# Performance work log

Measured on AMD Instinct MI355X. Metric: run time of the kernel, lower is better.

Reference implementation:

```python
import jax, jax.numpy as jnp
import numpy as np

H_LSTM = 80          # span-encoder LSTM hidden
SPAN_DIM = 4 * H_LSTM  # 320
ADU_DIM = 256        # han_out_size
HEADS = 3
HAN_HID = 256
CTX_DIM = 200


def lstm(x, W_ih, W_hh, b, reverse=False):
    # x: [T, B, In] -> hidden states [T, B, H]; torch gate order i,f,g,o
    H = W_hh.shape[1]
    B = x.shape[1]

    def step(carry, xt):
        h, c = carry
        z = xt @ W_ih.T + h @ W_hh.T + b
        i, f, g, o = jnp.split(z, 4, axis=-1)
        c = jax.nn.sigmoid(f) * c + jax.nn.sigmoid(i) * jnp.tanh(g)
        h = jax.nn.sigmoid(o) * jnp.tanh(c)
        return (h, c), h

    init = (jnp.zeros((B, H), x.dtype), jnp.zeros((B, H), x.dtype))
    _, hs = jax.lax.scan(step, init, x, reverse=reverse)
    return hs


def span_rep(seq, spans):
    # seq [L, 2H], spans [..., 2] -> [..., 4H]
    f, bwd = seq[:, :H_LSTM], seq[:, H_LSTM:]
    i, j = spans[..., 0], spans[..., 1]
    fi1, fj = f[i - 1], f[j]
    bi, bj1 = bwd[i], bwd[j + 1]
    return jnp.concatenate([fj - fi1, bi - bj1, fi1, bj1], axis=-1)


def gat_metapath(h, src, dst, emask, W, a_l, a_r, bias):
    # single-metapath GATConv (dgl semantics): h [A, Din], W [K, Din, D]
    A = h.shape[0]
    hp = jnp.einsum('ad,kdo->ako', h, W)  # [A,K,D]
    e = jax.nn.leaky_relu(jnp.einsum('eko,ko->ek', hp[src], a_l)
                          + jnp.einsum('eko,ko->ek', hp[dst], a_r), 0.2)
    e = jnp.where(emask[:, None], e, -1e9)
    m = jax.ops.segment_max(e, dst, num_segments=A)           # [A,K]
    ex = jnp.where(emask[:, None], jnp.exp(e - m[dst]), 0.0)
    den = jax.ops.segment_sum(ex, dst, num_segments=A)
    alpha = ex / jnp.maximum(den[dst], 1e-9)                  # edge softmax per dst
    out = jax.ops.segment_sum(alpha[:, :, None] * hp[src], dst, num_segments=A)
    out = jax.nn.elu(out + bias)                              # [A,K,D]
    return out.reshape(A, -1)                                 # [A, K*D]


def attn_pool(feats, vals, mask, W1, b1, W2, b2):
    # tiny MLP -> Softmax over axis 0 over the kept (masked) set
    s = jnp.maximum(feats @ W1 + b1, 0.0) @ W2 + b2           # [N,1]
    s = jnp.where(mask[:, None], s, -1e9)
    a = jnp.where(mask[:, None], jax.nn.softmax(s, axis=0), 0.0)
    out = (a * vals).sum(0)
    return jnp.where(mask.any(), out, jnp.zeros_like(out))


def _forward(token_embed, info_scores,
             Wih_f, Whh_f, b_f, Wih_b, Whh_b, b_b,
             W_gat, a_l, a_r, b_gat, W_sem, b_sem, q_sem, W_pred, b_pred,
             W_adu1, b_adu1, W_adu2, b_adu2,
             W_inn1, b_inn1, W_inn2, b_inn2,
             W_int1, b_int1, W_int2, b_int2,
             Wih_c, Whh_c, b_c,
             comment_spans, adu_spans, adu_masks, local_masks,
             inner_src, inner_dst, inner_rel, inner_mask,
             inter_src, inter_dst, inter_rel, inter_mask):
    # bidirectional span encoder over frozen LF token embeddings
    x = token_embed.transpose(1, 0, 2)                        # [L, C, 768]
    hf = lstm(x, Wih_f, Whh_f, b_f)
    hb = lstm(x, Wih_b, Whh_b, b_b, reverse=True)
    span_enc = jnp.concatenate([hf, hb], -1).transpose(1, 0, 2)  # [C, L, 2H]

    def per_comment(seq, cspan, aspans, amask, lmask,
                    isrc, idst, irel, imask_e,
                    tsrc, tdst, trel, tmask_e, info):
        cemb = span_rep(seq, cspan)                           # [320]
        adus = span_rep(seq, aspans) * amask[:, None]         # [A, 320]
        A = adus.shape[0]
        # meta-paths: inner Attack, inner Support, inter AttackedBy(rev), inter SupportedBy(rev)
        srcs = jnp.stack([isrc, isrc, tdst, tdst])
        dsts = jnp.stack([idst, idst, tsrc, tsrc])
        masks = jnp.stack([imask_e & (irel == 0), imask_e & (irel == 1),
                           tmask_e & (trel == 0), tmask_e & (trel == 1)])
        z = jax.vmap(gat_metapath, in_axes=(None, 0, 0, 0, 0, 0, 0, 0))(
            adus, srcs, dsts, masks, W_gat, a_l, a_r, b_gat)  # [4, A, K*D]
        # semantic attention across meta-paths (masked mean over real nodes)
        w = jnp.tanh(z @ W_sem + b_sem) @ q_sem               # [4, A]
        w = (w * amask[None, :]).sum(1) / jnp.maximum(amask.sum(), 1)
        beta = jax.nn.softmax(w)                              # [4]
        zfin = jnp.einsum('m,mad->ad', beta, z)               # [A, K*D]
        adu_embeds = zfin @ W_pred + b_pred                   # [A, 256]
        # ADU attention pooling over locally-used ADUs
        feats = jnp.concatenate(
            [jnp.broadcast_to(cemb, (A, SPAN_DIM)), adu_embeds], -1)
        attended_adu = attn_pool(feats, adu_embeds, amask & lmask,
                                 W_adu1, b_adu1, W_adu2, b_adu2)

        def pair_attend(se, de, rel, me, W1, b1, W2, b2):
            # relation lut: Attack(0)->[0,1], Support(1)->[1,0]
            onehot = jnp.stack([rel, 1 - rel], -1).astype(adu_embeds.dtype)
            pe = jnp.concatenate([adu_embeds[se], adu_embeds[de], onehot], -1)  # [E,514]
            fp = jnp.concatenate(
                [jnp.broadcast_to(cemb, (pe.shape[0], SPAN_DIM)), pe], -1)
            return attn_pool(fp, pe, me, W1, b1, W2, b2)

        attended_inner = pair_attend(isrc, idst, irel, imask_e,
                                     W_inn1, b_inn1, W_inn2, b_inn2)
        # revert_inter_post_relations=True: embed = cat(emb[pair1], emb[pair0], rel)
        attended_inter = pair_attend(tdst, tsrc, trel, tmask_e,
                                     W_int1, b_int1, W_int2, b_int2)
        return jnp.concatenate([attended_adu, attended_inner, attended_inter,
                                info, cemb])                  # [1608]

    wo_ctx = jax.vmap(per_comment)(span_enc, comment_spans, adu_spans, adu_masks,
                                   local_masks, inner_src, inner_dst, inner_rel,
                                   inner_mask, inter_src, inter_dst, inter_rel,
                                   inter_mask, info_scores)   # [C, 1608]
    # comment compressor LSTM along the comment sequence (batch = 1)
    ctx = lstm(wo_ctx[:, None, :], Wih_c, Whh_c, b_c)[:, 0, :]  # [C, 200]
    return jnp.concatenate([ctx, wo_ctx], -1)                 # [C, 1808]


def setup_inputs():
    C, L, A, E, INFO = 64, 1024, 32, 48, 4
    key = jax.random.key(0)
    ks = iter(jax.random.split(key, 64))
    rng = np.random.default_rng(0)

    def u(shape):  # uniform init as in _weight_init, scaled for stability
        return jax.random.uniform(next(ks), shape, jnp.float32, -0.1, 0.1)

    token_embed = jax.random.normal(next(ks), (C, L, 768), jnp.float32)
    info_scores = jax.random.normal(next(ks), (C, INFO), jnp.float32)
    ci = rng.integers(1, L // 2, C)
    cj = rng.integers(L // 2, L - 2, C)
    comment_spans = jnp.stack([jnp.asarray(ci), jnp.asarray(cj)], 1).astype(jnp.int32)
    ai = rng.integers(1, L - 40, (C, A))
    adu_spans = jnp.stack([jnp.asarray(ai), jnp.asarray(ai + rng.integers(1, 30, (C, A)))], -1).astype(jnp.int32)
    adu_masks = jnp.ones((C, A), jnp.bool_)
    local_masks = jnp.asarray(rng.integers(0, 2, (C, A)) > 0)
    ei = lambda hi, shp: jnp.asarray(rng.integers(0, hi, shp), jnp.int32)
    eb = lambda shp: jnp.asarray(rng.integers(0, 2, shp) > 0)
    inp = dict(token_embed=token_embed, info_scores=info_scores,
               comment_spans=comment_spans, adu_spans=adu_spans,
               adu_masks=adu_masks, local_masks=local_masks,
               inner_src=ei(A, (C, E)), inner_dst=ei(A, (C, E)),
               inner_rel=ei(2, (C, E)), inner_mask=eb((C, E)),
               inter_src=ei(A, (C, E)), inter_dst=ei(A, (C, E)),
               inter_rel=ei(2, (C, E)), inter_mask=eb((C, E)))
    D_WO = SPAN_DIM + ADU_DIM * 5 + 4 + INFO  # 1608
    params = dict(
        Wih_f=u((4 * H_LSTM, 768)), Whh_f=u((4 * H_LSTM, H_LSTM)), b_f=u((4 * H_LSTM,)),
        Wih_b=u((4 * H_LSTM, 768)), Whh_b=u((4 * H_LSTM, H_LSTM)), b_b=u((4 * H_LSTM,)),
        W_gat=u((4, HEADS, SPAN_DIM, HAN_HID)), a_l=u((4, HEADS, HAN_HID)),
        a_r=u((4, HEADS, HAN_HID)), b_gat=u((4, HEADS, HAN_HID)),
        W_sem=u((HEADS * HAN_HID, 128)), b_sem=u((128,)), q_sem=u((128,)),
        W_pred=u((HEADS * HAN_HID, ADU_DIM)), b_pred=u((ADU_DIM,)),
        W_adu1=u((SPAN_DIM + ADU_DIM, 16)), b_adu1=u((16,)), W_adu2=u((16, 1)), b_adu2=u((1,)),
        W_inn1=u((SPAN_DIM + 2 * ADU_DIM + 2, 16)), b_inn1=u((16,)), W_inn2=u((16, 1)), b_inn2=u((1,)),
        W_int1=u((SPAN_DIM + 2 * ADU_DIM + 2, 16)), b_int1=u((16,)), W_int2=u((16, 1)), b_int2=u((1,)),
        Wih_c=u((4 * CTX_DIM, D_WO)), Whh_c=u((4 * CTX_DIM, CTX_DIM)), b_c=u((4 * CTX_DIM,)))
    inp.update(params)
    return inp


def reference(token_embed, info_scores,
              Wih_f, Whh_f, b_f, Wih_b, Whh_b, b_b,
              W_gat, a_l, a_r, b_gat, W_sem, b_sem, q_sem, W_pred, b_pred,
              W_adu1, b_adu1, W_adu2, b_adu2,
              W_inn1, b_inn1, W_inn2, b_inn2,
              W_int1, b_int1, W_int2, b_int2,
              Wih_c, Whh_c, b_c,
              comment_spans, adu_spans, adu_masks, local_masks,
              inner_src, inner_dst, inner_rel, inner_mask,
              inter_src, inter_dst, inter_rel, inter_mask):
    return _forward(token_embed, info_scores,
                    Wih_f, Whh_f, b_f, Wih_b, Whh_b, b_b,
                    W_gat, a_l, a_r, b_gat, W_sem, b_sem, q_sem, W_pred, b_pred,
                    W_adu1, b_adu1, W_adu2, b_adu2,
                    W_inn1, b_inn1, W_inn2, b_inn2,
                    W_int1, b_int1, W_int2, b_int2,
                    Wih_c, Whh_c, b_c,
                    comment_spans, adu_spans, adu_masks, local_masks,
                    inner_src, inner_dst, inner_rel, inner_mask,
                    inter_src, inter_dst, inter_rel, inter_mask)
```

## Files before the change

kernel.cpp:

```cpp
#include <hip/hip_runtime.h>
#include <hip/hip_bf16.h>
#include <hip/hip_fp16.h>
#include <stdint.h>

typedef unsigned int u32;
typedef unsigned short u16;
typedef __attribute__((ext_vector_type(8))) short short8;
typedef __attribute__((ext_vector_type(4))) float f32x4;
typedef _Float16 half2v __attribute__((ext_vector_type(2)));

#if defined(__has_builtin)
#if __has_builtin(__builtin_amdgcn_fdot2)
#define HAVE_FDOT2 1
#endif
#endif

__device__ __forceinline__ float bf2f_u(u32 lo16) { return __uint_as_float(lo16 << 16); }
__device__ __forceinline__ u32 f2bf_bits(float x) {
  u32 u = __float_as_uint(x);
  return (u + 0x7fffu + ((u >> 16) & 1u)) >> 16;
}
__device__ __forceinline__ u32 pk2bf(float x, float y) {
  return f2bf_bits(x) | (f2bf_bits(y) << 16);
}
__device__ __forceinline__ u32 pk2bf_tr(float x, float y) {
  return (__float_as_uint(y) & 0xffff0000u) | (__float_as_uint(x) >> 16);
}
__device__ __forceinline__ u32 pkh(float x, float y) {
  return (u32)__half_as_ushort(__float2half(x)) |
         ((u32)__half_as_ushort(__float2half(y)) << 16);
}
__device__ __forceinline__ float dot2h(u32 w, u32 h, float acc) {
#ifdef HAVE_FDOT2
  return __builtin_amdgcn_fdot2(__builtin_bit_cast(half2v, w), __builtin_bit_cast(half2v, h),
                                acc, false);
#else
  union { u32 u; __half2 h2; } uw, uh;
  uw.u = w; uh.u = h;
  float2 wf = __half22float2(uw.h2);
  float2 hf = __half22float2(uh.h2);
  return acc + wf.x * hf.x + wf.y * hf.y;
#endif
}
__device__ __forceinline__ float sigf(float x) { return 1.0f / (1.0f + __expf(-x)); }
__device__ __forceinline__ float tanhf_fast(float x) {
  float ax = fabsf(x);
  float e = __expf(-2.0f * ax);
  float t = (1.0f - e) / (1.0f + e);
  return x < 0.0f ? -t : t;
}
__device__ __forceinline__ float eluf(float x) { return x > 0.0f ? x : __expf(x) - 1.0f; }
__device__ __forceinline__ float lreluf(float x) { return x > 0.0f ? x : 0.2f * x; }

__device__ __forceinline__ int maskmode(const void* am) { return (*(const u32*)am) > 0xFFu; }
__device__ __forceinline__ int ldmask(const void* p, int i, int mb) {
  return mb ? (int)((const unsigned char*)p)[i] : ((const int*)p)[i];
}

__global__ void k_marker(float* out) { out[0] = 12345.0f; }

__global__ void k_prep(const float* __restrict__ Wgat, const float* __restrict__ al,
                       const float* __restrict__ ar, float* __restrict__ alproj,
                       float* __restrict__ arproj) {
  int idx = blockIdx.x * 256 + threadIdx.x;
  if (idx >= 3840) return;
  int mk = idx / 320, d = idx % 320;
  const float* wrow = Wgat + ((size_t)mk * 320 + d) * 256;
  const float* alp = al + mk * 256;
  const float* arp = ar + mk * 256;
  float sa = 0.f, sb = 0.f;
  for (int o = 0; o < 256; ++o) {
    float w = wrow[o];
    sa += w * alp[o];
    sb += w * arp[o];
  }
  alproj[idx] = sa;
  arproj[idx] = sb;
}

__global__ void k_pack(const float* __restrict__ whhc, uint4* __restrict__ wt4) {
  int idx = blockIdx.x * 256 + threadIdx.x;
  if (idx >= 20000) return;
  int k4 = idx / 800, r = idx % 800;
  const float* p = whhc + r * 200 + k4 * 8;
  wt4[idx] = (uint4){pkh(p[0], p[1]), pkh(p[2], p[3]), pkh(p[4], p[5]), pkh(p[6], p[7])};
}

__global__ void k_packemb(const float* __restrict__ emb, u32* __restrict__ dst) {
  const float4* s = (const float4*)emb;
  uint2* d = (uint2*)dst;
  const int n = 12582912;
  for (int i = blockIdx.x * blockDim.x + threadIdx.x; i < n; i += gridDim.x * blockDim.x) {
    float4 v = s[i];
    d[i] = (uint2){pk2bf_tr(v.x, v.y), pk2bf_tr(v.z, v.w)};
  }
}

__global__ void k_packw(const float* __restrict__ Wf, const float* __restrict__ Wb,
                        u32* __restrict__ dst) {
  int idx = blockIdx.x * 256 + threadIdx.x;
  if (idx >= 245760) return;
  int n = idx / 384, q = (idx % 384) * 2;
  const float* src = (n < 320) ? (Wf + (size_t)n * 768) : (Wb + (size_t)(n - 320) * 768);
  dst[idx] = pk2bf_tr(src[q], src[q + 1]);
}

__global__ __launch_bounds__(256) void k_gemm_in(
    const float* __restrict__ emb, const float* __restrict__ Wf, const float* __restrict__ Wb,
    const float* __restrict__ biasf, const float* __restrict__ biasb, float* __restrict__ Z) {
  __shared__ u16 Albs[128 * 40];
  __shared__ u16 Blbs[128 * 40];
  __shared__ float bias_l[128];
  const int tid = threadIdx.x;
  const int n0 = blockIdx.x * 128;
  const int m0 = blockIdx.y * 128;

  if (tid < 128) {
    int ng = n0 + tid;
    bias_l[tid] = (ng < 320) ? biasf[ng] : biasb[ng - 320];
  }
  const int srow = tid >> 1, shalf = tid & 1;
  const float* asrc = emb + (size_t)(m0 + srow) * 768 + shalf * 16;
  const int ngb = n0 + srow;
  const float* bsrc =
      ((ngb < 320) ? (Wf + (size_t)ngb * 768) : (Wb + (size_t)(ngb - 320) * 768)) + shalf * 16;
  u32* aw = (u32*)&Albs[srow * 40 + shalf * 16];
  u32* bw = (u32*)&Blbs[srow * 40 + shalf * 16];

  const int lane = tid & 63;
  const int lr = lane & 15, sub = lane >> 4;
  const int wv = tid >> 6, wm = wv >> 1, wn = wv & 1;
  const u16* abase = &Albs[(wm * 64 + lr) * 40 + sub * 8];
  const u16* bbase = &Blbs[(wn * 64 + lr) * 40 + sub * 8];

  f32x4 acc[4][4];
#pragma unroll
  for (int i = 0; i < 4; ++i)
#pragma unroll
    for (int j = 0; j < 4; ++j) acc[i][j] = (f32x4)(0.f);

  float4 a0, a1, a2, a3, b0, b1, b2, b3;
  u32 pra[8], prb[8];
  a0 = *(const float4*)(asrc + 0); a1 = *(const float4*)(asrc + 4);
  a2 = *(const float4*)(asrc + 8); a3 = *(const float4*)(asrc + 12);
  b0 = *(const float4*)(bsrc + 0); b1 = *(const float4*)(bsrc + 4);
  b2 = *(const float4*)(bsrc + 8); b3 = *(const float4*)(bsrc + 12);
  pra[0] = pk2bf_tr(a0.x, a0.y); pra[1] = pk2bf_tr(a0.z, a0.w);
  pra[2] = pk2bf_tr(a1.x, a1.y); pra[3] = pk2bf_tr(a1.z, a1.w);
  pra[4] = pk2bf_tr(a2.x, a2.y); pra[5] = pk2bf_tr(a2.z, a2.w);
  pra[6] = pk2bf_tr(a3.x, a3.y); pra[7] = pk2bf_tr(a3.z, a3.w);
  prb[0] = pk2bf_tr(b0.x, b0.y); prb[1] = pk2bf_tr(b0.z, b0.w);
  prb[2] = pk2bf_tr(b1.x, b1.y); prb[3] = pk2bf_tr(b1.z, b1.w);
  prb[4] = pk2bf_tr(b2.x, b2.y); prb[5] = pk2bf_tr(b2.z, b2.w);
  prb[6] = pk2bf_tr(b3.x, b3.y); prb[7] = pk2bf_tr(b3.z, b3.w);

  for (int it = 0; it < 24; ++it) {
    __syncthreads();
#pragma unroll
    for (int q = 0; q < 8; ++q) { aw[q] = pra[q]; bw[q] = prb[q]; }
    __syncthreads();
    const bool more = (it + 1 < 24);
    if (more) {
      const int k0 = (it + 1) * 32;
      a0 = *(const float4*)(asrc + k0); a1 = *(const float4*)(asrc + k0 + 4);
      a2 = *(const float4*)(asrc + k0 + 8); a3 = *(const float4*)(asrc + k0 + 12);
      b0 = *(const float4*)(bsrc + k0); b1 = *(const float4*)(bsrc + k0 + 4);
      b2 = *(const float4*)(bsrc + k0 + 8); b3 = *(const float4*)(bsrc + k0 + 12);
    }
    short8 bfr[4];
#pragma unroll
    for (int nf = 0; nf < 4; ++nf) bfr[nf] = *(const short8*)(bbase + nf * 640);
#pragma unroll
    for (int mf = 0; mf < 4; ++mf) {
      short8 af = *(const short8*)(abase + mf * 640);
#pragma unroll
      for (int nf = 0; nf < 4; ++nf)
        acc[mf][nf] = __builtin_amdgcn_mfma_f32_16x16x32_bf16(af, bfr[nf], acc[mf][nf], 0, 0, 0);
    }
    if (more) {
      pra[0] = pk2bf_tr(a0.x, a0.y); pra[1] = pk2bf_tr(a0.z, a0.w);
      pra[2] = pk2bf_tr(a1.x, a1.y); pra[3] = pk2bf_tr(a1.z, a1.w);
      pra[4] = pk2bf_tr(a2.x, a2.y); pra[5] = pk2bf_tr(a2.z, a2.w);
      pra[6] = pk2bf_tr(a3.x, a3.y); pra[7] = pk2bf_tr(a3.z, a3.w);
      prb[0] = pk2bf_tr(b0.x, b0.y); prb[1] = pk2bf_tr(b0.z, b0.w);
      prb[2] = pk2bf_tr(b1.x, b1.y); prb[3] = pk2bf_tr(b1.z, b1.w);
      prb[4] = pk2bf_tr(b2.x, b2.y); prb[5] = pk2bf_tr(b2.z, b2.w);
      prb[6] = pk2bf_tr(b3.x, b3.y); prb[7] = pk2bf_tr(b3.z, b3.w);
    }
  }
#pragma unroll
  for (int mf = 0; mf < 4; ++mf) {
#pragma unroll
    for (int nf = 0; nf < 4; ++nf) {
      int col = wn * 64 + nf * 16 + lr;
      float bias = bias_l[col];
      size_t mrow = (size_t)m0 + wm * 64 + mf * 16 + sub * 4;
#pragma unroll
      for (int j = 0; j < 4; ++j)
        Z[(mrow + j) * 640 + n0 + col] = acc[mf][nf][j] + bias;
    }
  }
}

__global__ __launch_bounds__(256) void k_gemm_in2(
    const u32* __restrict__ ebf, const u32* __restrict__ wbf, const float* __restrict__ biasf,
    const float* __restrict__ biasb, float* __restrict__ Z) {
  __shared__ u16 Albs[128 * 40];
  __shared__ u16 Blbs[128 * 40];
  __shared__ float bias_l[128];
  const int tid = threadIdx.x;
  const int n0 = blockIdx.x * 128;
  const int m0 = blockIdx.y * 128;

  if (tid < 128) {
    int ng = n0 + tid;
    bias_l[tid] = (ng < 320) ? biasf[ng] : biasb[ng - 320];
  }
  const int srow = tid >> 1, shalf = tid & 1;
  const uint4* ea = (const uint4*)ebf + (size_t)(m0 + srow) * 96 + shalf * 2;
  const uint4* eb = (const uint4*)wbf + (size_t)(n0 + srow) * 96 + shalf * 2;
  uint4* aw4 = (uint4*)&Albs[srow * 40 + shalf * 16];
  uint4* bw4 = (uint4*)&Blbs[srow * 40 + shalf * 16];

  const int lane = tid & 63;
  const int lr = lane & 15, sub = lane >> 4;
  const int wv = tid >> 6, wm = wv >> 1, wn = wv & 1;
  const u16* abase = &Albs[(wm * 64 + lr) * 40 + sub * 8];
  const u16* bbase = &Blbs[(wn * 64 + lr) * 40 + sub * 8];

  f32x4 acc[4][4];
#pragma unroll
  for (int i = 0; i < 4; ++i)
#pragma unroll
    for (int j = 0; j < 4; ++j) acc[i][j] = (f32x4)(0.f);

  uint4 pa0 = ea[0], pa1 = ea[1], pb0 = eb[0], pb1 = eb[1];
  for (int it = 0; it < 24; ++it) {
    __syncthreads();
    aw4[0] = pa0; aw4[1] = pa1;
    bw4[0] = pb0; bw4[1] = pb1;
    __syncthreads();
    if (it + 1 < 24) {
      pa0 = ea[(it + 1) * 4]; pa1 = ea[(it + 1) * 4 + 1];
      pb0 = eb[(it + 1) * 4]; pb1 = eb[(it + 1) * 4 + 1];
    }
    short8 bfr[4];
#pragma unroll
    for (int nf = 0; nf < 4; ++nf) bfr[nf] = *(const short8*)(bbase + nf * 640);
#pragma unroll
    for (int mf = 0; mf < 4; ++mf) {
      short8 af = *(const short8*)(abase + mf * 640);
#pragma unroll
      for (int nf = 0; nf < 4; ++nf)
        acc[mf][nf] = __builtin_amdgcn_mfma_f32_16x16x32_bf16(af, bfr[nf], acc[mf][nf], 0, 0, 0);
    }
  }
#pragma unroll
  for (int mf = 0; mf < 4; ++mf) {
#pragma unroll
    for (int nf = 0; nf < 4; ++nf) {
      int col = wn * 64 + nf * 16 + lr;
      float bias = bias_l[col];
      size_t mrow = (size_t)m0 + wm * 64 + mf * 16 + sub * 4;
#pragma unroll
      for (int j = 0; j < 4; ++j)
        Z[(mrow + j) * 640 + n0 + col] = acc[mf][nf][j] + bias;
    }
  }
}

__global__ __launch_bounds__(320, 1) void k_lstm_tok(const float* __restrict__ Z,
                                                     const float* __restrict__ Whhf,
                                                     const float* __restrict__ Whhb,
                                                     float* __restrict__ hf,
                                                     float* __restrict__ hb) {
  __shared__ uint2 wq[20 * 320];
  __shared__ alignas(16) u32 hpkA[40];
  __shared__ alignas(16) u32 hpkB[40];
  const int tid = threadIdx.x;
  const int c = blockIdx.x >> 1;
  const int dir = blockIdx.x & 1;
  const float* Whh = dir ? Whhb : Whhf;
  float* hout = dir ? hb : hf;

  for (int idx = tid; idx < 20 * 320; idx += 320) {
    int k4 = idx / 320, r = idx % 320;
    const float* p = Whh + (size_t)r * 80 + k4 * 4;
    wq[idx] = (uint2){pkh(p[0], p[1]), pkh(p[2], p[3])};
  }
  if (tid < 40) hpkA[tid] = 0;
  __syncthreads();

  const int u = tid >> 2, g = tid & 3;
  const int r = g * 80 + u;
  const int lb = tid & 60;
  const uint2* wcol = wq + r;
  uint2 wv0 = wcol[0], wv1 = wcol[320], wv2 = wcol[640], wv3 = wcol[960];
  uint2 wv4 = wcol[1280], wv5 = wcol[1600], wv6 = wcol[1920], wv7 = wcol[2240];
  uint2 wv8 = wcol[2560], wv9 = wcol[2880], wv10 = wcol[3200], wv11 = wcol[3520];
  uint2 wv12 = wcol[3840], wv13 = wcol[4160], wv14 = wcol[4480], wv15 = wcol[4800];
  uint2 wv16 = wcol[5120], wv17 = wcol[5440], wv18 = wcol[5760], wv19 = wcol[6080];
  asm volatile("" : "+v"(wv0.x), "+v"(wv0.y), "+v"(wv1.x), "+v"(wv1.y), "+v"(wv2.x),
                    "+v"(wv2.y), "+v"(wv3.x), "+v"(wv3.y), "+v"(wv4.x), "+v"(wv4.y),
                    "+v"(wv5.x), "+v"(wv5.y), "+v"(wv6.x), "+v"(wv6.y), "+v"(wv7.x),
                    "+v"(wv7.y), "+v"(wv8.x), "+v"(wv8.y), "+v"(wv9.x), "+v"(wv9.y));
  asm volatile("" : "+v"(wv10.x), "+v"(wv10.y), "+v"(wv11.x), "+v"(wv11.y), "+v"(wv12.x),
                    "+v"(wv12.y), "+v"(wv13.x), "+v"(wv13.y), "+v"(wv14.x), "+v"(wv14.y),
                    "+v"(wv15.x), "+v"(wv15.y), "+v"(wv16.x), "+v"(wv16.y), "+v"(wv17.x),
                    "+v"(wv17.y), "+v"(wv18.x), "+v"(wv18.y), "+v"(wv19.x), "+v"(wv19.y));

  const int sgn = dir ? -1 : 1;
  const int t0 = dir ? 1023 : 0;
  const float* zb = Z + (size_t)c * 1024 * 640 + dir * 320 + r;
  float zc = zb[(size_t)t0 * 640];
  float zn = zb[(size_t)(t0 + sgn) * 640];
  float cst = 0.f;
  const u32* cur = hpkA;
  u32* nxt = hpkB;
  float* hbase = hout + (size_t)c * 1024 * 80 + u;

  for (int t = 0; t < 1024; ++t) {
    const int tt = t0 + sgn * t;
    float zp = 0.f;
    if (t + 2 < 1024) zp = zb[(size_t)(t0 + sgn * (t + 2)) * 640];
    float a0 = zc, a1 = 0.f, a2 = 0.f, a3 = 0.f;
    {
      uint4 h0 = *(const uint4*)&cur[0];
      a0 = dot2h(wv0.x, h0.x, a0); a1 = dot2h(wv0.y, h0.y, a1);
      a2 = dot2h(wv1.x, h0.z, a2); a3 = dot2h(wv1.y, h0.w, a3);
      uint4 h1 = *(const uint4*)&cur[4];
      a0 = dot2h(wv2.x, h1.x, a0); a1 = dot2h(wv2.y, h1.y, a1);
      a2 = dot2h(wv3.x, h1.z, a2); a3 = dot2h(wv3.y, h1.w, a3);
      uint4 h2 = *(const uint4*)&cur[8];
      a0 = dot2h(wv4.x, h2.x, a0); a1 = dot2h(wv4.y, h2.y, a1);
      a2 = dot2h(wv5.x, h2.z, a2); a3 = dot2h(wv5.y, h2.w, a3);
      uint4 h3 = *(const uint4*)&cur[12];
      a0 = dot2h(wv6.x, h3.x, a0); a1 = dot2h(wv6.y, h3.y, a1);
      a2 = dot2h(wv7.x, h3.z, a2); a3 = dot2h(wv7.y, h3.w, a3);
      uint4 h4 = *(const uint4*)&cur[16];
      a0 = dot2h(wv8.x, h4.x, a0); a1 = dot2h(wv8.y, h4.y, a1);
      a2 = dot2h(wv9.x, h4.z, a2); a3 = dot2h(wv9.y, h4.w, a3);
      uint4 h5 = *(const uint4*)&cur[20];
      a0 = dot2h(wv10.x, h5.x, a0); a1 = dot2h(wv10.y, h5.y, a1);
      a2 = dot2h(wv11.x, h5.z, a2); a3 = dot2h(wv11.y, h5.w, a3);
      uint4 h6 = *(const uint4*)&cur[24];
      a0 = dot2h(wv12.x, h6.x, a0); a1 = dot2h(wv12.y, h6.y, a1);
      a2 = dot2h(wv13.x, h6.z, a2); a3 = dot2h(wv13.y, h6.w, a3);
      uint4 h7 = *(const uint4*)&cur[28];
      a0 = dot2h(wv14.x, h7.x, a0); a1 = dot2h(wv14.y, h7.y, a1);
      a2 = dot2h(wv15.x, h7.z, a2); a3 = dot2h(wv15.y, h7.w, a3);
      uint4 h8 = *(const uint4*)&cur[32];
      a0 = dot2h(wv16.x, h8.x, a0); a1 = dot2h(wv16.y, h8.y, a1);
      a2 = dot2h(wv17.x, h8.z, a2); a3 = dot2h(wv17.y, h8.w, a3);
      uint4 h9 = *(const uint4*)&cur[36];
      a0 = dot2h(wv18.x, h9.x, a0); a1 = dot2h(wv18.y, h9.y, a1);
      a2 = dot2h(wv19.x, h9.z, a2); a3 = dot2h(wv19.y, h9.w, a3);
    }
    float asum = (a0 + a1) + (a2 + a3);
    float zi = __shfl(asum, lb + 0, 64);
    float zf_ = __shfl(asum, lb + 1, 64);
    float zg = __shfl(asum, lb + 2, 64);
    float zo = __shfl(asum, lb + 3, 64);
    float iv = sigf(zi);
    float fv = sigf(zf_);
    float gv = tanhf_fast(zg);
    float ov = sigf(zo);
    cst = fv * cst + iv * gv;
    float h = ov * tanhf_fast(cst);
    if (g == 0) {
      ((u16*)nxt)[u] = (u16)__half_as_ushort(__float2half(h));
      hbase[(size_t)tt * 80] = h;
    }
    zc = zn; zn = zp;
    const u32* tc = cur; cur = nxt; nxt = (u32*)tc;
    __syncthreads();
  }
}

__device__ __forceinline__ float span_val(const float* __restrict__ hf,
                                          const float* __restrict__ hb, int c, int i, int j,
                                          int d) {
  size_t base = (size_t)c * 1024 * 80;
  if (d < 80) return hf[base + (size_t)j * 80 + d] - hf[base + (size_t)(i - 1) * 80 + d];
  if (d < 160) return hb[base + (size_t)i * 80 + (d - 80)] - hb[base + (size_t)(j + 1) * 80 + (d - 80)];
  if (d < 240) return hf[base + (size_t)(i - 1) * 80 + (d - 160)];
  return hb[base + (size_t)(j + 1) * 80 + (d - 240)];
}

__global__ __launch_bounds__(256) void k_span(const float* __restrict__ hf,
                                              const float* __restrict__ hb,
                                              const int* __restrict__ cspan,
                                              const int* __restrict__ aspan,
                                              const void* __restrict__ amask,
                                              float* __restrict__ adus, float* __restrict__ cembo) {
  const int c = blockIdx.x, tid = threadIdx.x;
  const int mb = maskmode(amask);
  int ci = cspan[c * 2], cj = cspan[c * 2 + 1];
  for (int d = tid; d < 320; d += 256) cembo[c * 320 + d] = span_val(hf, hb, c, ci, cj, d);
  for (int idx = tid; idx < 32 * 320; idx += 256) {
    int a = idx / 320, d = idx % 320;
    float v = 0.f;
    if (ldmask(amask, c * 32 + a, mb)) {
      int ai = aspan[(c * 32 + a) * 2], aj = aspan[(c * 32 + a) * 2 + 1];
      v = span_val(hf, hb, c, ai, aj, d);
    }
    adus[(size_t)c * 10240 + idx] = v;
  }
}

__global__ __launch_bounds__(256) void k_gat(
    const float* __restrict__ adus_ws, const float* __restrict__ alproj,
    const float* __restrict__ arproj, const float* __restrict__ Wgat,
    const float* __restrict__ bgat, const int* __restrict__ isrc, const int* __restrict__ idst,
    const int* __restrict__ irel, const void* __restrict__ imask, const int* __restrict__ tsrc,
    const int* __restrict__ tdst, const int* __restrict__ trel, const void* __restrict__ tmask,
    const void* __restrict__ amdet, float* __restrict__ zgat) {
  __shared__ float adus_l[32][321];
  __shared__ float Wst[16][64];
  __shared__ float hp_t[32][66];
  __shared__ float sl_l[96], sr_l[96];
  __shared__ float e_l[144], alpha_l[144], mx_l[96], den_l[96];
  __shared__ int src_l[48], dst_l[48], valid_l[48];
  const int c = blockIdx.x >> 2, m = blockIdx.x & 3;
  const int tid = threadIdx.x;
  const int mb = maskmode(amdet);

  if (tid < 48) {
    int e = tid, s, d, r, mk;
    if (m < 2) {
      s = isrc[c * 48 + e]; d = idst[c * 48 + e]; r = irel[c * 48 + e];
      mk = ldmask(imask, c * 48 + e, mb);
    } else {
      s = tdst[c * 48 + e]; d = tsrc[c * 48 + e]; r = trel[c * 48 + e];
      mk = ldmask(tmask, c * 48 + e, mb);
    }
    src_l[e] = s; dst_l[e] = d; valid_l[e] = (mk != 0) && (r == (m & 1));
  }
  for (int idx = tid; idx < 32 * 320; idx += 256)
    adus_l[idx / 320][idx % 320] = adus_ws[(size_t)c * 10240 + idx];
  __syncthreads();

  if (tid < 96) {
    int a = tid & 31, k = tid >> 5;
    const float* alp = alproj + (m * 3 + k) * 320;
    const float* arp = arproj + (m * 3 + k) * 320;
    float sa = 0.f, sb = 0.f;
    for (int d = 0; d < 320; ++d) {
      float v = adus_l[a][d];
      sa += v * alp[d];
      sb += v * arp[d];
    }
    sl_l[a * 3 + k] = sa;
    sr_l[a * 3 + k] = sb;
  }
  __syncthreads();
  if (tid < 144) {
    int e = tid % 48, k = tid / 48;
    float v = -1e30f;
    if (valid_l[e]) v = lreluf(sl_l[src_l[e] * 3 + k] + sr_l[dst_l[e] * 3 + k]);
    e_l[e * 3 + k] = v;
  }
  __syncthreads();
  if (tid < 96) {
    int a = tid & 31, k = tid >> 5;
    float mx = -1e30f;
    for (int e = 0; e < 48; ++e)
      if (valid_l[e] && dst_l[e] == a) mx = fmaxf(mx, e_l[e * 3 + k]);
    float den = 0.f;
    for (int e = 0; e < 48; ++e)
      if (valid_l[e] && dst_l[e] == a) den += __expf(e_l[e * 3 + k] - mx);
    mx_l[a * 3 + k] = mx;
    den_l[a * 3 + k] = den;
  }
  __syncthreads();
  if (tid < 144) {
    int e = tid % 48, k = tid / 48;
    float v = 0.f;
    if (valid_l[e]) {
      int d = dst_l[e];
      v = __expf(e_l[e * 3 + k] - mx_l[d * 3 + k]) / fmaxf(den_l[d * 3 + k], 1e-9f);
    }
    alpha_l[e * 3 + k] = v;
  }
  __syncthreads();

  const int ag = tid >> 3, og = tid & 7;
  for (int k = 0; k < 3; ++k) {
    for (int ot = 0; ot < 4; ++ot) {
      float acc[8];
#pragma unroll
      for (int i = 0; i < 8; ++i) acc[i] = 0.f;
      for (int dt = 0; dt < 320; dt += 16) {
        {
          int dd = tid >> 4, oq = (tid & 15) * 4;
          const float* p = Wgat + ((size_t)((m * 3 + k) * 320 + dt + dd)) * 256 + ot * 64 + oq;
          float4 v = *(const float4*)p;
          Wst[dd][oq + 0] = v.x;
          Wst[dd][oq + 1] = v.y;
          Wst[dd][oq + 2] = v.z;
          Wst[dd][oq + 3] = v.w;
        }
        __syncthreads();
#pragma unroll
        for (int dd = 0; dd < 16; ++dd) {
          float av = adus_l[ag][dt + dd];
          const float4 w0 = *(const float4*)(&Wst[dd][og * 8]);
          const float4 w1 = *(const float4*)(&Wst[dd][og * 8 + 4]);
          acc[0] += av * w0.x; acc[1] += av * w0.y; acc[2] += av * w0.z; acc[3] += av * w0.w;
          acc[4] += av * w1.x; acc[5] += av * w1.y; acc[6] += av * w1.z; acc[7] += av * w1.w;
        }
        __syncthreads();
      }
#pragma unroll
      for (int i = 0; i < 8; ++i) hp_t[ag][og * 8 + i] = acc[i];
      __syncthreads();
      float oacc[8];
#pragma unroll
      for (int i = 0; i < 8; ++i) oacc[i] = 0.f;
      for (int e = 0; e < 48; ++e) {
        if (valid_l[e] && dst_l[e] == ag) {
          float alv = alpha_l[e * 3 + k];
          int s = src_l[e];
#pragma unroll
          for (int i = 0; i < 8; ++i) oacc[i] += alv * hp_t[s][og * 8 + i];
        }
      }
#pragma unroll
      for (int i = 0; i < 8; ++i) {
        int o = ot * 64 + og * 8 + i;
        float v = eluf(oacc[i] + bgat[(m * 3 + k) * 256 + o]);
        zgat[((size_t)(c * 4 + m) * 32 + ag) * 768 + k * 256 + o] = v;
      }
      __syncthreads();
    }
  }
}

__global__ __launch_bounds__(256) void k_sem(const float* __restrict__ zgat,
                                             const float* __restrict__ Wsem,
                                             const float* __restrict__ bsem,
                                             const float* __restrict__ qsem,
                                             const void* __restrict__ amask,
                                             float* __restrict__ wsem) {
  __shared__ float Wst[64][128];
  __shared__ float zl[32][64];
  __shared__ float wred[256];
  __shared__ float war[32];
  const int c = blockIdx.x >> 2, m = blockIdx.x & 3;
  const int tid = threadIdx.x;
  const int mb = maskmode(amask);
  const int a = tid >> 3, hg = tid & 7;
  float acc[16];
#pragma unroll
  for (int i = 0; i < 16; ++i) acc[i] = 0.f;
  const float* zbase = zgat + (size_t)(c * 4 + m) * 32 * 768;
  for (int jt = 0; jt < 768; jt += 64) {
    for (int l = 0; l < 8; ++l) {
      int f4 = l * 256 + tid;
      int row = f4 >> 5, c4 = (f4 & 31) * 4;
      *(float4*)&Wst[row][c4] = *(const float4*)(Wsem + (size_t)(jt + row) * 128 + c4);
    }
    for (int l = 0; l < 2; ++l) {
      int f4 = l * 256 + tid;
      int row = f4 >> 4, c4 = (f4 & 15) * 4;
      *(float4*)&zl[row][c4] = *(const float4*)(zbase + (size_t)row * 768 + jt + c4);
    }
    __syncthreads();
    for (int j = 0; j < 64; ++j) {
      float zv = zl[a][j];
      const float* wp = &Wst[j][hg * 16];
#pragma unroll
      for (int i = 0; i < 16; ++i) acc[i] += zv * wp[i];
    }
    __syncthreads();
  }
  float wp_ = 0.f;
#pragma unroll
  for (int i = 0; i < 16; ++i) {
    int h = hg * 16 + i;
    wp_ += tanhf_fast(acc[i] + bsem[h]) * qsem[h];
  }
  wred[tid] = wp_;
  __syncthreads();
  if (tid < 32) {
    float s = 0.f;
    for (int q = 0; q < 8; ++q) s += wred[tid * 8 + q];
    war[tid] = s;
  }
  __syncthreads();
  if (tid == 0) {
    float s = 0.f;
    int cnt = 0;
    for (int aa = 0; aa < 32; ++aa)
      if (ldmask(amask, c * 32 + aa, mb)) { s += war[aa]; cnt++; }
    wsem[c * 4 + m] = s / (float)(cnt > 1 ? cnt : 1);
  }
}

__global__ __launch_bounds__(256) void k_comment(
    const float* __restrict__ zgat, const float* __restrict__ wsem,
    const float* __restrict__ cemb_ws, const float* __restrict__ Wpred,
    const float* __restrict__ bpred, const float* __restrict__ Wadu1,
    const float* __restrict__ badu1, const float* __restrict__ Wadu2,
    const float* __restrict__ badu2, const float* __restrict__ Winn1,
    const float* __restrict__ binn1, const float* __restrict__ Winn2,
    const float* __restrict__ binn2, const float* __restrict__ Wint1,
    const float* __restrict__ bint1, const float* __restrict__ Wint2,
    const float* __restrict__ bint2, const float* __restrict__ info,
    const void* __restrict__ amask, const void* __restrict__ lmask,
    const int* __restrict__ isrc, const int* __restrict__ idst,
    const int* __restrict__ irel, const void* __restrict__ imask, const int* __restrict__ tsrc,
    const int* __restrict__ tdst, const int* __restrict__ trel, const void* __restrict__ tmask,
    float* __restrict__ woctx, float* __restrict__ dout) {
  __shared__ float zf[32][133];
  __shared__ float ae[32][257];
  __shared__ float cemb_l[320];
  __shared__ float beta_l[4];
  __shared__ float pred_l[48][16];
  __shared__ float sE[48], alE[48];
  __shared__ int seL[48], deL[48], relL[48], mskL[48];
  __shared__ float wredA[256];
  __shared__ float sA[32], alA[32];
  __shared__ int mskA[32];
  const int c = blockIdx.x, tid = threadIdx.x;
  const int mb = maskmode(amask);

  if (tid == 0) {
    float w0 = wsem[c * 4], w1 = wsem[c * 4 + 1], w2 = wsem[c * 4 + 2], w3 = wsem[c * 4 + 3];
    float mx = fmaxf(fmaxf(w0, w1), fmaxf(w2, w3));
    float e0 = __expf(w0 - mx), e1 = __expf(w1 - mx), e2 = __expf(w2 - mx), e3 = __expf(w3 - mx);
    float s = e0 + e1 + e2 + e3;
    beta_l[0] = e0 / s; beta_l[1] = e1 / s; beta_l[2] = e2 / s; beta_l[3] = e3 / s;
  }
  for (int d = tid; d < 320; d += 256) cemb_l[d] = cemb_ws[c * 320 + d];
  __syncthreads();

  const int ag = tid >> 5;
  const int og = tid & 31;
  float acc[4][8];
#pragma unroll
  for (int i = 0; i < 4; ++i)
#pragma unroll
    for (int j = 0; j < 8; ++j) acc[i][j] = 0.f;
  const float b0 = beta_l[0], b1 = beta_l[1], b2 = beta_l[2], b3 = beta_l[3];
  const float* zc0 = zgat + (size_t)(c * 4 + 0) * 32 * 768;
  const float* zc1 = zgat + (size_t)(c * 4 + 1) * 32 * 768;
  const float* zc2 = zgat + (size_t)(c * 4 + 2) * 32 * 768;
  const float* zc3 = zgat + (size_t)(c * 4 + 3) * 32 * 768;
  for (int jt = 0; jt < 768; jt += 128) {
    for (int l = 0; l < 16; ++l) {
      int idx = l * 256 + tid;
      int a = idx >> 7, j = idx & 127;
      size_t off = (size_t)a * 768 + jt + j;
      zf[a][j] = b0 * zc0[off] + b1 * zc1[off] + b2 * zc2[off] + b3 * zc3[off];
    }
    __syncthreads();
    for (int j = 0; j < 128; ++j) {
      const float* wp = Wpred + (size_t)(jt + j) * 256 + og * 8;
      float4 w0v = *(const float4*)wp;
      float4 w1v = *(const float4*)(wp + 4);
      float w8[8] = {w0v.x, w0v.y, w0v.z, w0v.w, w1v.x, w1v.y, w1v.z, w1v.w};
      float z0 = zf[ag * 4 + 0][j], z1 = zf[ag * 4 + 1][j];
      float z2 = zf[ag * 4 + 2][j], z3 = zf[ag * 4 + 3][j];
#pragma unroll
      for (int jj = 0; jj < 8; ++jj) {
        acc[0][jj] += z0 * w8[jj];
        acc[1][jj] += z1 * w8[jj];
        acc[2][jj] += z2 * w8[jj];
        acc[3][jj] += z3 * w8[jj];
      }
    }
    __syncthreads();
  }
#pragma unroll
  for (int i = 0; i < 4; ++i)
#pragma unroll
    for (int jj = 0; jj < 8; ++jj)
      ae[ag * 4 + i][og * 8 + jj] = acc[i][jj] + bpred[og * 8 + jj];
  __syncthreads();

  {
    const int a = tid >> 3, hg = tid & 7;
    float sacc = 0.f;
    for (int hh = 0; hh < 2; ++hh) {
      int h = hg * 2 + hh;
      float d = badu1[h];
      for (int dd = 0; dd < 320; ++dd) d += cemb_l[dd] * Wadu1[dd * 16 + h];
      for (int dd = 0; dd < 256; ++dd) d += ae[a][dd] * Wadu1[(320 + dd) * 16 + h];
      sacc += fmaxf(d, 0.f) * Wadu2[h];
    }
    wredA[tid] = sacc;
  }
  __syncthreads();
  if (tid < 32) {
    float s = badu2[0];
    for (int q = 0; q < 8; ++q) s += wredA[tid * 8 + q];
    sA[tid] = s;
    mskA[tid] = (ldmask(amask, c * 32 + tid, mb) != 0) && (ldmask(lmask, c * 32 + tid, mb) != 0);
  }
  __syncthreads();
  if (tid == 0) {
    float mx = -1e30f;
    int any = 0;
    for (int a = 0; a < 32; ++a)
      if (mskA[a]) { any = 1; mx = fmaxf(mx, sA[a]); }
    float s = 0.f;
    for (int a = 0; a < 32; ++a) {
      float v = mskA[a] ? __expf(sA[a] - mx) : 0.f;
      alA[a] = v;
      s += v;
    }
    if (any)
      for (int a = 0; a < 32; ++a) alA[a] /= s;
  }
  __syncthreads();
  {
    int o = tid;
    float v = 0.f;
    for (int a = 0; a < 32; ++a) v += alA[a] * ae[a][o];
    woctx[c * 1608 + o] = v;
    dout[(size_t)c * 1808 + 200 + o] = v;
  }
  __syncthreads();

  for (int pp = 0; pp < 2; ++pp) {
    const float *W1, *b1v, *W2, *b2v;
    const int *seP, *deP, *relP;
    const void* mskP;
    int outoff;
    if (pp == 0) {
      W1 = Winn1; b1v = binn1; W2 = Winn2; b2v = binn2;
      seP = isrc; deP = idst; relP = irel; mskP = imask; outoff = 256;
    } else {
      W1 = Wint1; b1v = bint1; W2 = Wint2; b2v = bint2;
      seP = tdst; deP = tsrc; relP = trel; mskP = tmask; outoff = 770;
    }
    if (tid < 48) {
      seL[tid] = seP[c * 48 + tid];
      deL[tid] = deP[c * 48 + tid];
      relL[tid] = relP[c * 48 + tid];
      mskL[tid] = (ldmask(mskP, c * 48 + tid, mb) != 0);
    }
    __syncthreads();
    for (int u = tid; u < 768; u += 256) {
      int e = u >> 4, h = u & 15;
      int se = seL[e], de = deL[e];
      float rel = (float)relL[e];
      float d = b1v[h];
      for (int dd = 0; dd < 320; ++dd) d += cemb_l[dd] * W1[dd * 16 + h];
      for (int dd = 0; dd < 256; ++dd) d += ae[se][dd] * W1[(320 + dd) * 16 + h];
      for (int dd = 0; dd < 256; ++dd) d += ae[de][dd] * W1[(576 + dd) * 16 + h];
      d += rel * W1[832 * 16 + h] + (1.f - rel) * W1[833 * 16 + h];
      pred_l[e][h] = fmaxf(d, 0.f) * W2[h];
    }
    __syncthreads();
    if (tid < 48) {
      float s = b2v[0];
      for (int h = 0; h < 16; ++h) s += pred_l[tid][h];
      sE[tid] = s;
    }
    __syncthreads();
    if (tid == 0) {
      float mx = -1e30f;
      int any = 0;
      for (int e = 0; e < 48; ++e)
        if (mskL[e]) { any = 1; mx = fmaxf(mx, sE[e]); }
      float s = 0.f;
      for (int e = 0; e < 48; ++e) {
        float v = mskL[e] ? __expf(sE[e] - mx) : 0.f;
        alE[e] = v;
        s += v;
      }
      if (any)
        for (int e = 0; e < 48; ++e) alE[e] /= s;
    }
    __syncthreads();
    for (int dim = tid; dim < 514; dim += 256) {
      float v = 0.f;
      for (int e = 0; e < 48; ++e) {
        float alv = alE[e];
        float pe;
        if (dim < 256) pe = ae[seL[e]][dim];
        else if (dim < 512) pe = ae[deL[e]][dim - 256];
        else if (dim == 512) pe = (float)relL[e];
        else pe = 1.f - (float)relL[e];
        v += alv * pe;
      }
      woctx[c * 1608 + outoff + dim] = v;
      dout[(size_t)c * 1808 + 200 + outoff + dim] = v;
    }
    __syncthreads();
  }

  if (tid < 4) {
    float v = info[c * 4 + tid];
    woctx[c * 1608 + 1284 + tid] = v;
    dout[(size_t)c * 1808 + 200 + 1284 + tid] = v;
  }
  for (int d = tid; d < 320; d += 256) {
    float v = cemb_l[d];
    woctx[c * 1608 + 1288 + d] = v;
    dout[(size_t)c * 1808 + 200 + 1288 + d] = v;
  }
}

__global__ __launch_bounds__(256) void k_ctx_in(const float* __restrict__ woctx,
                                                const float* __restrict__ Wihc,
                                                const float* __restrict__ bc,
                                                float* __restrict__ xc) {
  __shared__ float woc[64][133];
  __shared__ float Wst[8][128];
  const int r0 = blockIdx.x * 8;
  const int tid = threadIdx.x;
  const int t = tid & 63, rg = tid >> 6;
  float a0 = 0.f, a1 = 0.f;
  for (int d0 = 0; d0 < 1608; d0 += 128) {
    int jn = 1608 - d0;
    if (jn > 128) jn = 128;
    for (int l = 0; l < 32; ++l) {
      int idx = l * 256 + tid;
      int tt = idx >> 7, j = idx & 127;
      woc[tt][j] = (j < jn) ? woctx[(size_t)tt * 1608 + d0 + j] : 0.f;
    }
    {
      int rr = tid >> 5, jb = tid & 31;
      for (int q = 0; q < 4; ++q) {
        int jj = jb * 4 + q;
        Wst[rr][jj] = (jj < jn) ? Wihc[(size_t)(r0 + rr) * 1608 + d0 + jj] : 0.f;
      }
    }
    __syncthreads();
    for (int j = 0; j < 128; ++j) {
      float x = woc[t][j];
      a0 += x * Wst[rg * 2 + 0][j];
      a1 += x * Wst[rg * 2 + 1][j];
    }
    __syncthreads();
  }
  int r = r0 + rg * 2;
  xc[t * 800 + r] = a0 + bc[r];
  xc[t * 800 + r + 1] = a1 + bc[r + 1];
}

__global__ __launch_bounds__(832) void k_ctx_rec(const float* __restrict__ xc,
                                                 const uint4* __restrict__ wt4,
                                                 float* __restrict__ dout) {
  __shared__ alignas(16) u32 hl2[100];
  __shared__ float zc[800];
  const int tid = threadIdx.x;
  if (tid < 100) hl2[tid] = 0;
  float cst = 0.f;
  __syncthreads();
  for (int t = 0; t < 64; ++t) {
    if (tid < 800) {
      float a0 = xc[t * 800 + tid], a1 = 0.f, a2 = 0.f, a3 = 0.f;
#pragma unroll 5
      for (int k4 = 0; k4 < 25; ++k4) {
        uint4 wv = wt4[(size_t)k4 * 800 + tid];
        uint4 hq = *(const uint4*)&hl2[k4 * 4];
        a0 = dot2h(wv.x, hq.x, a0);
        a1 = dot2h(wv.y, hq.y, a1);
        a2 = dot2h(wv.z, hq.z, a2);
        a3 = dot2h(wv.w, hq.w, a3);
      }
      zc[tid] = (a0 + a1) + (a2 + a3);
    }
    __syncthreads();
    if (tid < 200) {
      float iv = sigf(zc[tid]);
      float fv = sigf(zc[200 + tid]);
      float gv = tanhf_fast(zc[400 + tid]);
      float ov = sigf(zc[600 + tid]);
      cst = fv * cst + iv * gv;
      float h = ov * tanhf_fast(cst);
      ((u16*)hl2)[tid] = __half_as_ushort(__float2half(h));
      dout[(size_t)t * 1808 + tid] = h;
    }
    __syncthreads();
  }
}

extern "C" void kernel_launch(void* const* d_in, const int* in_sizes, int n_in, void* d_out,
                              int out_size, void* d_ws, size_t ws_size, hipStream_t stream) {
  const float* emb = (const float*)d_in[0];
  const float* info = (const float*)d_in[1];
  const int* cspan = (const int*)d_in[2];
  const int* aspan = (const int*)d_in[3];
  const void* amask = d_in[4];
  const void* lmask = d_in[5];
  const int* isrc = (const int*)d_in[6];
  const int* idst = (const int*)d_in[7];
  const int* irel = (const int*)d_in[8];
  const void* imask = d_in[9];
  const int* tsrc = (const int*)d_in[10];
  const int* tdst = (const int*)d_in[11];
  const int* trel = (const int*)d_in[12];
  const void* tmask = d_in[13];
  const float* Wihf = (const float*)d_in[14];
  const float* Whhf = (const float*)d_in[15];
  const float* bfv = (const float*)d_in[16];
  const float* Wihb = (const float*)d_in[17];
  const float* Whhb = (const float*)d_in[18];
  const float* bbv = (const float*)d_in[19];
  const float* Wgat = (const float*)d_in[20];
  const float* al = (const float*)d_in[21];
  const float* ar = (const float*)d_in[22];
  const float* bgat = (const float*)d_in[23];
  const float* Wsem = (const float*)d_in[24];
  const float* bsem = (const float*)d_in[25];
  const float* qsem = (const float*)d_in[26];
  const float* Wpred = (const float*)d_in[27];
  const float* bpred = (const float*)d_in[28];
  const float* Wadu1 = (const float*)d_in[29];
  const float* badu1 = (const float*)d_in[30];
  const float* Wadu2 = (const float*)d_in[31];
  const float* badu2 = (const float*)d_in[32];
  const float* Winn1 = (const float*)d_in[33];
  const float* binn1 = (const float*)d_in[34];
  const float* Winn2 = (const float*)d_in[35];
  const float* binn2 = (const float*)d_in[36];
  const float* Wint1 = (const float*)d_in[37];
  const float* bint1 = (const float*)d_in[38];
  const float* Wint2 = (const float*)d_in[39];
  const float* bint2 = (const float*)d_in[40];
  const float* Wihc = (const float*)d_in[41];
  const float* Whhc = (const float*)d_in[42];
  const float* bc = (const float*)d_in[43];
  float* out = (float*)d_out;
  float* ws = (float*)d_ws;

  const size_t OFF_Z = 0;
  const size_t OFF_HF = OFF_Z + (size_t)65536 * 640;
  const size_t OFF_HB = OFF_HF + (size_t)64 * 1024 * 80;
  const size_t OFF_ZG = OFF_HB + (size_t)64 * 1024 * 80;
  const size_t OFF_AD = OFF_ZG + (size_t)64 * 4 * 32 * 768;
  const size_t OFF_CE = OFF_AD + (size_t)64 * 32 * 320;
  const size_t OFF_WS4 = OFF_CE + 64 * 320;
  const size_t OFF_ALP = OFF_WS4 + 256;
  const size_t OFF_ARP = OFF_ALP + 3840;
  const size_t OFF_WO = OFF_ARP + 3840;
  const size_t OFF_XC = OFF_WO + (size_t)64 * 1608;
  const size_t OFF_WT = OFF_XC + (size_t)64 * 800;
  const size_t TOTAL = OFF_WT + 80000;
  const size_t OFF_EBF = TOTAL;
  const size_t OFF_WBF = OFF_EBF + (size_t)65536 * 384;
  const size_t TOTAL_EXT = OFF_WBF + 245760;

  if (n_in < 44 || ws_size < TOTAL * sizeof(float)) {
    k_marker<<<1, 1, 0, stream>>>(out);
    return;
  }
  const bool ext = ws_size >= TOTAL_EXT * sizeof(float);

  k_prep<<<15, 256, 0, stream>>>(Wgat, al, ar, ws + OFF_ALP, ws + OFF_ARP);
  k_pack<<<79, 256, 0, stream>>>(Whhc, (uint4*)(ws + OFF_WT));
  dim3 g1(5, 512);
  if (ext) {
    k_packemb<<<2048, 256, 0, stream>>>(emb, (u32*)(ws + OFF_EBF));
    k_packw<<<960, 256, 0, stream>>>(Wihf, Wihb, (u32*)(ws + OFF_WBF));
    k_gemm_in2<<<g1, 256, 0, stream>>>((const u32*)(ws + OFF_EBF), (const u32*)(ws + OFF_WBF),
                                       bfv, bbv, ws + OFF_Z);
  } else {
    k_gemm_in<<<g1, 256, 0, stream>>>(emb, Wihf, Wihb, bfv, bbv, ws + OFF_Z);
  }
  k_lstm_tok<<<128, 320, 0, stream>>>(ws + OFF_Z, Whhf, Whhb, ws + OFF_HF, ws + OFF_HB);
  k_span<<<64, 256, 0, stream>>>(ws + OFF_HF, ws + OFF_HB, cspan, aspan, amask, ws + OFF_AD,
                                 ws + OFF_CE);
  k_gat<<<256, 256, 0, stream>>>(ws + OFF_AD, ws + OFF_ALP, ws + OFF_ARP, Wgat, bgat, isrc, idst,
                                 irel, imask, tsrc, tdst, trel, tmask, amask, ws + OFF_ZG);
  k_sem<<<256, 256, 0, stream>>>(ws + OFF_ZG, Wsem, bsem, qsem, amask, ws + OFF_WS4);
  k_comment<<<64, 256, 0, stream>>>(ws + OFF_ZG, ws + OFF_WS4, ws + OFF_CE, Wpred, bpred, Wadu1,
                                    badu1, Wadu2, badu2, Winn1, binn1, Winn2, binn2, Wint1, bint1,
                                    Wint2, bint2, info, amask, lmask, isrc, idst, irel, imask,
                                    tsrc, tdst, trel, tmask, ws + OFF_WO, out);
  k_ctx_in<<<100, 256, 0, stream>>>(ws + OFF_WO, Wihc, bc, ws + OFF_XC);
  k_ctx_rec<<<1, 832, 0, stream>>>(ws + OFF_XC, (const uint4*)(ws + OFF_WT), out);
}
```

Baseline: 1.909 ms.

## Permute Z gate columns for coalesced LSTM loads; warp-parallel k_prep reduction

The input-projection GEMMs now write Z with gate columns interleaved per hidden unit (u*4+g), so each LSTM thread reads its per-step preactivation at offset tid, which makes the loads contiguous instead of strided by gate. The LSTM weight staging loop is reordered for more contiguous global reads, and the register-pinning asm barriers are removed. k_prep changes from one thread per dot product to one wavefront per dot product with a shuffle reduction over 960 blocks. The GEMM epilogue stores become scattered, and dropping the asm pins risks the compiler spilling or reloading the weight registers.

```diff
diff --git a/kernel.cpp b/kernel.cpp
--- a/kernel.cpp
+++ b/kernel.cpp
@@ -57,25 +57,41 @@
   return mb ? (int)((const unsigned char*)p)[i] : ((const int*)p)[i];
 }
 
+__device__ __forceinline__ int zperm(int n) {
+  int dir = n >= 320;
+  int nn = n - (dir ? 320 : 0);
+  int g = nn / 80, u = nn % 80;
+  return dir * 320 + u * 4 + g;
+}
+
 __global__ void k_marker(float* out) { out[0] = 12345.0f; }
 
-__global__ void k_prep(const float* __restrict__ Wgat, const float* __restrict__ al,
-                       const float* __restrict__ ar, float* __restrict__ alproj,
-                       float* __restrict__ arproj) {
-  int idx = blockIdx.x * 256 + threadIdx.x;
-  if (idx >= 3840) return;
-  int mk = idx / 320, d = idx % 320;
+__global__ __launch_bounds__(256) void k_prep(const float* __restrict__ Wgat,
+                                              const float* __restrict__ al,
+                                              const float* __restrict__ ar,
+                                              float* __restrict__ alproj,
+                                              float* __restrict__ arproj) {
+  int w = blockIdx.x * 4 + (threadIdx.x >> 6);
+  int lane = threadIdx.x & 63;
+  if (w >= 3840) return;
+  int mk = w / 320, d = w % 320;
   const float* wrow = Wgat + ((size_t)mk * 320 + d) * 256;
   const float* alp = al + mk * 256;
   const float* arp = ar + mk * 256;
   float sa = 0.f, sb = 0.f;
-  for (int o = 0; o < 256; ++o) {
-    float w = wrow[o];
-    sa += w * alp[o];
-    sb += w * arp[o];
-  }
-  alproj[idx] = sa;
-  arproj[idx] = sb;
+#pragma unroll
+  for (int q = 0; q < 4; ++q) {
+    int o = lane + q * 64;
+    float wv = wrow[o];
+    sa += wv * alp[o];
+    sb += wv * arp[o];
+  }
+#pragma unroll
+  for (int off = 32; off; off >>= 1) {
+    sa += __shfl_down(sa, off, 64);
+    sb += __shfl_down(sb, off, 64);
+  }
+  if (lane == 0) { alproj[w] = sa; arproj[w] = sb; }
 }
 
 __global__ void k_pack(const float* __restrict__ whhc, uint4* __restrict__ wt4) {
@@ -192,12 +208,13 @@
   for (int mf = 0; mf < 4; ++mf) {
 #pragma unroll
     for (int nf = 0; nf < 4; ++nf) {
-      int col = wn * 64 + nf * 16 + lr;
-      float bias = bias_l[col];
+      int col = n0 + wn * 64 + nf * 16 + lr;
+      float bias = bias_l[wn * 64 + nf * 16 + lr];
+      int pc = zperm(col);
       size_t mrow = (size_t)m0 + wm * 64 + mf * 16 + sub * 4;
 #pragma unroll
       for (int j = 0; j < 4; ++j)
-        Z[(mrow + j) * 640 + n0 + col] = acc[mf][nf][j] + bias;
+        Z[(mrow + j) * 640 + pc] = acc[mf][nf][j] + bias;
     }
   }
 }
@@ -259,12 +276,13 @@
   for (int mf = 0; mf < 4; ++mf) {
 #pragma unroll
     for (int nf = 0; nf < 4; ++nf) {
-      int col = wn * 64 + nf * 16 + lr;
-      float bias = bias_l[col];
+      int col = n0 + wn * 64 + nf * 16 + lr;
+      float bias = bias_l[wn * 64 + nf * 16 + lr];
+      int pc = zperm(col);
       size_t mrow = (size_t)m0 + wm * 64 + mf * 16 + sub * 4;
 #pragma unroll
       for (int j = 0; j < 4; ++j)
-        Z[(mrow + j) * 640 + n0 + col] = acc[mf][nf][j] + bias;
+        Z[(mrow + j) * 640 + pc] = acc[mf][nf][j] + bias;
     }
   }
 }
@@ -284,9 +302,9 @@
   float* hout = dir ? hb : hf;
 
   for (int idx = tid; idx < 20 * 320; idx += 320) {
-    int k4 = idx / 320, r = idx % 320;
-    const float* p = Whh + (size_t)r * 80 + k4 * 4;
-    wq[idx] = (uint2){pkh(p[0], p[1]), pkh(p[2], p[3])};
+    int r2 = idx / 20, k4 = idx % 20;
+    const float* p = Whh + (size_t)r2 * 80 + k4 * 4;
+    wq[k4 * 320 + r2] = (uint2){pkh(p[0], p[1]), pkh(p[2], p[3])};
   }
   if (tid < 40) hpkA[tid] = 0;
   __syncthreads();
@@ -300,18 +318,10 @@
   uint2 wv8 = wcol[2560], wv9 = wcol[2880], wv10 = wcol[3200], wv11 = wcol[3520];
   uint2 wv12 = wcol[3840], wv13 = wcol[4160], wv14 = wcol[4480], wv15 = wcol[4800];
   uint2 wv16 = wcol[5120], wv17 = wcol[5440], wv18 = wcol[5760], wv19 = wcol[6080];
-  asm volatile("" : "+v"(wv0.x), "+v"(wv0.y), "+v"(wv1.x), "+v"(wv1.y), "+v"(wv2.x),
-                    "+v"(wv2.y), "+v"(wv3.x), "+v"(wv3.y), "+v"(wv4.x), "+v"(wv4.y),
-                    "+v"(wv5.x), "+v"(wv5.y), "+v"(wv6.x), "+v"(wv6.y), "+v"(wv7.x),
-                    "+v"(wv7.y), "+v"(wv8.x), "+v"(wv8.y), "+v"(wv9.x), "+v"(wv9.y));
-  asm volatile("" : "+v"(wv10.x), "+v"(wv10.y), "+v"(wv11.x), "+v"(wv11.y), "+v"(wv12.x),
-                    "+v"(wv12.y), "+v"(wv13.x), "+v"(wv13.y), "+v"(wv14.x), "+v"(wv14.y),
-                    "+v"(wv15.x), "+v"(wv15.y), "+v"(wv16.x), "+v"(wv16.y), "+v"(wv17.x),
-                    "+v"(wv17.y), "+v"(wv18.x), "+v"(wv18.y), "+v"(wv19.x), "+v"(wv19.y));
 
   const int sgn = dir ? -1 : 1;
   const int t0 = dir ? 1023 : 0;
-  const float* zb = Z + (size_t)c * 1024 * 640 + dir * 320 + r;
+  const float* zb = Z + (size_t)c * 1024 * 640 + dir * 320 + tid;
   float zc = zb[(size_t)t0 * 640];
   float zn = zb[(size_t)(t0 + sgn) * 640];
   float cst = 0.f;
@@ -952,7 +962,7 @@
   }
   const bool ext = ws_size >= TOTAL_EXT * sizeof(float);
 
-  k_prep<<<15, 256, 0, stream>>>(Wgat, al, ar, ws + OFF_ALP, ws + OFF_ARP);
+  k_prep<<<960, 256, 0, stream>>>(Wgat, al, ar, ws + OFF_ALP, ws + OFF_ARP);
   k_pack<<<79, 256, 0, stream>>>(Whhc, (uint4*)(ws + OFF_WT));
   dim3 g1(5, 512);
   if (ext) {
```

After: 1.976 ms. +3.5%, slower.
